# Optimization experiments

Hardware: AMD Instinct MI355X
Metric: run time of the kernel (lower is better)

Reference implementation:

```python
import math
import jax, jax.numpy as jnp
import numpy as np

NUM_HEADS = 16
D_MODEL = 1024
WINDOW = 512


def alibi_slopes(num_heads):
    # 1 / ((2**8)**((i+1)/num_heads))  for i in range(num_heads)
    x = (2.0 ** 8) ** (1.0 / num_heads)
    return jnp.asarray([1.0 / x ** (i + 1) for i in range(num_heads)], dtype=jnp.float32)


def setup_inputs() -> dict:
    key = jax.random.key(0)
    k1, k2 = jax.random.split(key)
    x = jax.random.normal(k1, (1, 4096, D_MODEL), dtype=jnp.float32)
    # scale weight like a trained init so softmax isn't saturated
    w_kqv = jax.random.normal(k2, (D_MODEL, 3 * D_MODEL), dtype=jnp.float32) * 0.02
    return {"x": x, "w_kqv": w_kqv}


def reference(x, w_kqv):
    B, S, D = x.shape
    H = NUM_HEADS
    hd = D // H
    scale = math.sqrt(D)  # module scales by sqrt(d_model), not sqrt(head_dim)

    kqv = x @ w_kqv                       # [B, S, 3D]
    k, q, v = jnp.split(kqv, 3, axis=-1)  # chunk order: key, query, value
    k = k.reshape(B, S, H, hd).transpose(0, 2, 1, 3)  # [B, H, S, hd]
    q = q.reshape(B, S, H, hd).transpose(0, 2, 1, 3)
    v = v.reshape(B, S, H, hd).transpose(0, 2, 1, 3)

    # ALiBi bias: m_h * (j - i)
    pos = jnp.arange(S)
    rel = pos[None, :] - pos[:, None]                  # [S, S] = x - y
    bias = alibi_slopes(H)[:, None, None] * rel.astype(jnp.float32)  # [H, S, S]

    score = jnp.einsum("bhqd,bhkd->bhqk", q, k) / scale + bias[None]

    # causal sliding-window mask: allow 0 <= i - j <= WINDOW
    dist = pos[:, None] - pos[None, :]                 # i - j
    mask = (dist >= 0) & (dist <= WINDOW)              # [S, S]
    score = jnp.where(mask[None, None], score, -jnp.inf)

    attn = jax.nn.softmax(score, axis=-1)
    out = jnp.einsum("bhqk,bhkd->bhqd", attn, v)       # [B, H, S, hd]
    out = out.transpose(0, 2, 1, 3).reshape(B, S, D)
    return out
```

## Files before the change

### kernel.cpp

```cpp
#include <hip/hip_runtime.h>
#include <hip/hip_bf16.h>

#define SEQ   4096
#define DM    1024
#define NH    16
#define HD    64
#define N3    3072
#define WIN   512

#define LOG2E 1.4426950408889634f

typedef __attribute__((ext_vector_type(8))) short short8;
typedef __attribute__((ext_vector_type(4))) short short4v;
typedef __attribute__((ext_vector_type(4))) float float4v;

__device__ __forceinline__ float bf16_bits_to_float(unsigned short u) {
  return __uint_as_float(((unsigned int)u) << 16);
}

typedef __attribute__((address_space(3))) void lds_void_t;
typedef __attribute__((address_space(1))) const void gbl_void_t;
__device__ __forceinline__ void async_copy16(void* lds_dst, const void* g_src) {
  __builtin_amdgcn_global_load_lds((gbl_void_t*)g_src, (lds_void_t*)lds_dst,
                                   16, 0, 0);
}

__device__ __forceinline__ int detect_fp32(const unsigned short* __restrict__ probe,
                                           float* red) {
  const int t = threadIdx.x;
  float mx = 0.0f;
#pragma unroll
  for (int p = 0; p < 8; ++p) {
    float v = bf16_bits_to_float(probe[(t * 8 + p) * 2]);
    if (v != v) v = 1e38f;
    mx = fmaxf(mx, fabsf(v));
  }
  red[t] = mx;
  __syncthreads();
  for (int s = 128; s > 0; s >>= 1) {
    if (t < s) red[t] = fmaxf(red[t], red[t + s]);
    __syncthreads();
  }
  const int fl = red[0] > 100.0f ? 1 : 0;
  __syncthreads();
  return fl;
}

__global__ __launch_bounds__(256) void prep(
    const void* __restrict__ x, const void* __restrict__ w,
    __hip_bfloat16* __restrict__ xb, __hip_bfloat16* __restrict__ wt) {
  __shared__ __hip_bfloat16 tile[64][66];
  __shared__ float red[256];
  const int t = threadIdx.x;
  if (blockIdx.x < 2048) {
    const int fl = detect_fp32((const unsigned short*)x, red);
    const int i0 = (blockIdx.x * 256 + t) * 8;
    if (fl) {
      const float* xf = (const float*)x + i0;
      float4 f0 = *(const float4*)(xf);
      float4 f1 = *(const float4*)(xf + 4);
      __hip_bfloat16 tmp[8];
      tmp[0] = __float2bfloat16(f0.x); tmp[1] = __float2bfloat16(f0.y);
      tmp[2] = __float2bfloat16(f0.z); tmp[3] = __float2bfloat16(f0.w);
      tmp[4] = __float2bfloat16(f1.x); tmp[5] = __float2bfloat16(f1.y);
      tmp[6] = __float2bfloat16(f1.z); tmp[7] = __float2bfloat16(f1.w);
      *(uint4*)&xb[i0] = *(const uint4*)tmp;
    } else {
      *(uint4*)&xb[i0] = *(const uint4*)((const __hip_bfloat16*)x + i0);
    }
  } else {
    const int bid = blockIdx.x - 2048;
    const int fl = detect_fp32((const unsigned short*)w, red);
    const int n0 = (bid % 48) * 64;
    const int k0 = (bid / 48) * 64;
    const int tx = t & 63, ty0 = t >> 6;
    if (fl) {
      const float* wf = (const float*)w;
#pragma unroll
      for (int p = 0; p < 16; ++p) {
        int row = ty0 + p * 4;
        tile[row][tx] = __float2bfloat16(wf[(k0 + row) * N3 + n0 + tx]);
      }
    } else {
      const __hip_bfloat16* wb = (const __hip_bfloat16*)w;
#pragma unroll
      for (int p = 0; p < 16; ++p) {
        int row = ty0 + p * 4;
        tile[row][tx] = wb[(k0 + row) * N3 + n0 + tx];
      }
    }
    __syncthreads();
#pragma unroll
    for (int r = 0; r < 2; ++r) {
      int oe = r * 2048 + t * 8;
      int nr = oe >> 6, kc = oe & 63;
      __hip_bfloat16 v[8];
#pragma unroll
      for (int e = 0; e < 8; ++e) v[e] = tile[kc + e][nr];
      *(uint4*)&wt[(n0 + nr) * DM + k0 + kc] = *(const uint4*)v;
    }
  }
}

__global__ __launch_bounds__(256) void gemm_kqv(
    const __hip_bfloat16* __restrict__ A,
    const __hip_bfloat16* __restrict__ BT,
    __hip_bfloat16* __restrict__ C) {
  __shared__ __align__(16) __hip_bfloat16 As[2][128 * 32];
  __shared__ __align__(16) __hip_bfloat16 Bs[2][128 * 32];
  const int m0 = blockIdx.y * 128;
  const int n0 = blockIdx.x * 128;
  const int t = threadIdx.x;
  const int wave = t >> 6, lane = t & 63;
  const int wm = wave >> 1, wn = wave & 1;
  const int l15 = lane & 15, quad = lane >> 4;

  const int srow0 = wave * 16 + (lane >> 2);
  const int scol  = (lane & 3) * 8;
  const int sbyte = wave * 1024 + lane * 16;

  float4v acc[4][4] = {};

  for (int k0 = 0; k0 < DM; k0 += 64) {
    __syncthreads();
#pragma unroll
    for (int half = 0; half < 2; ++half) {
      const int kk = k0 + half * 32;
#pragma unroll
      for (int r = 0; r < 2; ++r) {
        const int row = srow0 + r * 64;
        async_copy16((char*)As[half] + r * 4096 + sbyte,
                     &A[(m0 + row) * DM + kk + scol]);
        async_copy16((char*)Bs[half] + r * 4096 + sbyte,
                     &BT[(n0 + row) * DM + kk + scol]);
      }
    }
    __syncthreads();

#pragma unroll
    for (int half = 0; half < 2; ++half) {
      short8 a[4], b[4];
#pragma unroll
      for (int mi = 0; mi < 4; ++mi)
        a[mi] = *(const short8*)(&As[half][(wm * 64 + mi * 16 + l15) * 32 + quad * 8]);
#pragma unroll
      for (int ni = 0; ni < 4; ++ni)
        b[ni] = *(const short8*)(&Bs[half][(wn * 64 + ni * 16 + l15) * 32 + quad * 8]);
#pragma unroll
      for (int mi = 0; mi < 4; ++mi)
#pragma unroll
        for (int ni = 0; ni < 4; ++ni)
          acc[mi][ni] = __builtin_amdgcn_mfma_f32_16x16x32_bf16(
              a[mi], b[ni], acc[mi][ni], 0, 0, 0);
    }
  }

#pragma unroll
  for (int mi = 0; mi < 4; ++mi)
#pragma unroll
    for (int ni = 0; ni < 4; ++ni)
#pragma unroll
      for (int r = 0; r < 4; ++r) {
        int row = m0 + wm * 64 + mi * 16 + quad * 4 + r;
        int col = n0 + wn * 64 + ni * 16 + l15;
        C[row * N3 + col] = __float2bfloat16(acc[mi][ni][r]);
      }
}

__global__ __launch_bounds__(256, 4) void attn(
    const __hip_bfloat16* __restrict__ kqv,
    const unsigned short* __restrict__ xprobe,
    void* __restrict__ out) {
  __shared__ __align__(16) __hip_bfloat16 Ks[64 * 72];
  __shared__ __align__(16) __hip_bfloat16 Vt[80 * 68];
  __shared__ __align__(16) __hip_bfloat16 Ps[64 * 72];
  __shared__ float red[256];

  const int fl = detect_fp32(xprobe, red);
  const int h  = blockIdx.y;
  const int i0 = blockIdx.x * 64;
  const int t    = threadIdx.x;
  const int wave = t >> 6, lane = t & 63;
  const int l15 = lane & 15, quad = lane >> 4;
  const float slope2 = exp2f(-0.5f * (float)(h + 1)) * LOG2E;
  const float qscale = LOG2E / 32.0f;

  for (int idx = t; idx < 16 * 68; idx += 256) {
    int rr = idx / 68, cc = idx - rr * 68;
    ((unsigned short*)Vt)[(64 + rr) * 68 + cc] = (rr == 0) ? 0x3F80 : 0;
  }

  short8 aq[2];
#pragma unroll
  for (int ks2 = 0; ks2 < 2; ++ks2)
    aq[ks2] = *(const short8*)&kqv[(i0 + wave * 16 + l15) * N3 + DM + h * HD +
                                   ks2 * 32 + quad * 8];

  float4v o[5] = {};

  const int jlo  = max(0, i0 - WIN);
  const int nblk = (i0 + 64 - jlo) >> 6;

  for (int b = 0; b < nblk; ++b) {
    const int j0 = jlo + b * 64;
    __syncthreads();
    for (int c = t; c < 512; c += 256) {
      int row = c >> 3, d0 = (c & 7) * 8;
      *(uint4*)&Ks[row * 72 + d0] =
          *(const uint4*)&kqv[(j0 + row) * N3 + h * HD + d0];
    }
    {
      int rp = t >> 3, d0 = (t & 7) * 8, r0 = rp * 2;
      uint4 va = *(const uint4*)&kqv[(j0 + r0) * N3 + 2 * DM + h * HD + d0];
      uint4 vb = *(const uint4*)&kqv[(j0 + r0 + 1) * N3 + 2 * DM + h * HD + d0];
      const unsigned short* pa = (const unsigned short*)&va;
      const unsigned short* pb = (const unsigned short*)&vb;
#pragma unroll
      for (int e = 0; e < 8; ++e) {
        unsigned int pack = (unsigned int)pa[e] | ((unsigned int)pb[e] << 16);
        *(unsigned int*)&Vt[(d0 + e) * 68 + r0] = pack;
      }
    }
    __syncthreads();

    float4v sacc[4] = {};
#pragma unroll
    for (int ks2 = 0; ks2 < 2; ++ks2)
#pragma unroll
      for (int nt = 0; nt < 4; ++nt) {
        short8 bk = *(const short8*)&Ks[(nt * 16 + l15) * 72 + ks2 * 32 + quad * 8];
        sacc[nt] = __builtin_amdgcn_mfma_f32_16x16x32_bf16(aq[ks2], bk, sacc[nt], 0, 0, 0);
      }

#pragma unroll
    for (int r = 0; r < 4; ++r) {
      const int i = i0 + wave * 16 + quad * 4 + r;
#pragma unroll
      for (int nt = 0; nt < 4; ++nt) {
        const int j = j0 + nt * 16 + l15;
        const int rel = i - j;
        float x = sacc[nt][r] * qscale + slope2 * (float)(j - i);
        x = (rel >= 0 && rel <= WIN) ? x : -200.0f;
        Ps[(wave * 16 + quad * 4 + r) * 72 + nt * 16 + l15] =
            __float2bfloat16(exp2f(x));
      }
    }

#pragma unroll
    for (int ks = 0; ks < 64; ks += 32) {
      short8 ap = *(const short8*)&Ps[(wave * 16 + l15) * 72 + ks + quad * 8];
#pragma unroll
      for (int dt = 0; dt < 5; ++dt) {
        const __hip_bfloat16* vp = &Vt[(dt * 16 + l15) * 68 + ks + quad * 8];
        short4v v0 = *(const short4v*)vp;
        short4v v1 = *(const short4v*)(vp + 4);
        short8 bv;
#pragma unroll
        for (int e = 0; e < 4; ++e) { bv[e] = v0[e]; bv[4 + e] = v1[e]; }
        o[dt] = __builtin_amdgcn_mfma_f32_16x16x32_bf16(ap, bv, o[dt], 0, 0, 0);
      }
    }
  }

#pragma unroll
  for (int r = 0; r < 4; ++r) {
    const float l = __shfl(o[4][r], quad * 16, 64);
    const float inv_l = 1.0f / l;
    const int row = i0 + wave * 16 + quad * 4 + r;
#pragma unroll
    for (int dt = 0; dt < 4; ++dt) {
      const int idx = row * DM + h * HD + dt * 16 + l15;
      const float v = o[dt][r] * inv_l;
      if (fl) ((float*)out)[idx] = v;
      else    ((__hip_bfloat16*)out)[idx] = __float2bfloat16(v);
    }
  }
}

extern "C" void kernel_launch(void* const* d_in, const int* in_sizes, int n_in,
                              void* d_out, int out_size, void* d_ws, size_t ws_size,
                              hipStream_t stream) {
  char* ws = (char*)d_ws;
  __hip_bfloat16* wt  = (__hip_bfloat16*)(ws + 4096);
  __hip_bfloat16* kqv = (__hip_bfloat16*)(ws + 4096 + 6291456);
  __hip_bfloat16* xb  = (__hip_bfloat16*)d_out;

  hipLaunchKernelGGL(prep, dim3(2048 + 768), dim3(256), 0, stream,
                     d_in[0], d_in[1], xb, wt);
  hipLaunchKernelGGL(gemm_kqv, dim3(24, 32), dim3(256), 0, stream, xb, wt, kqv);
  hipLaunchKernelGGL(attn, dim3(64, 16), dim3(256), 0, stream,
                     kqv, (const unsigned short*)d_in[0], d_out);
}
```

Baseline: 152.0 us.

## Prefetch next K/V tile into registers and interleave query-block order

The attention loop now loads the next K and V tiles from global memory into registers while the current tile is being computed, so global latency overlaps with MFMA and softmax work. Query blocks are permuted across blockIdx.x to balance the uneven per-block work near the sequence start. The bias and mask math is strength-reduced to an incremental fmaf plus an unsigned compare, and the V fragment assembly uses a shufflevector. The register prefetch raises per-thread register use, which could lower occupancy under the launch bound of 4.

```diff
diff --git a/kernel.cpp b/kernel.cpp
--- a/kernel.cpp
+++ b/kernel.cpp
@@ -25,6 +25,7 @@
                                    16, 0, 0);
 }
 
+template <int NT>
 __device__ __forceinline__ int detect_fp32(const unsigned short* __restrict__ probe,
                                            float* red) {
   const int t = threadIdx.x;
@@ -37,7 +38,7 @@
   }
   red[t] = mx;
   __syncthreads();
-  for (int s = 128; s > 0; s >>= 1) {
+  for (int s = NT / 2; s > 0; s >>= 1) {
     if (t < s) red[t] = fmaxf(red[t], red[t + s]);
     __syncthreads();
   }
@@ -53,7 +54,7 @@
   __shared__ float red[256];
   const int t = threadIdx.x;
   if (blockIdx.x < 2048) {
-    const int fl = detect_fp32((const unsigned short*)x, red);
+    const int fl = detect_fp32<256>((const unsigned short*)x, red);
     const int i0 = (blockIdx.x * 256 + t) * 8;
     if (fl) {
       const float* xf = (const float*)x + i0;
@@ -70,7 +71,7 @@
     }
   } else {
     const int bid = blockIdx.x - 2048;
-    const int fl = detect_fp32((const unsigned short*)w, red);
+    const int fl = detect_fp32<256>((const unsigned short*)w, red);
     const int n0 = (bid % 48) * 64;
     const int k0 = (bid / 48) * 64;
     const int tx = t & 63, ty0 = t >> 6;
@@ -176,14 +177,16 @@
   __shared__ __align__(16) __hip_bfloat16 Ps[64 * 72];
   __shared__ float red[256];
 
-  const int fl = detect_fp32(xprobe, red);
+  const int fl = detect_fp32<256>(xprobe, red);
   const int h  = blockIdx.y;
-  const int i0 = blockIdx.x * 64;
+  const int bx = blockIdx.x;
+  const int i0 = 64 * ((bx & 7) * 8 + (bx >> 3));
   const int t    = threadIdx.x;
   const int wave = t >> 6, lane = t & 63;
   const int l15 = lane & 15, quad = lane >> 4;
-  const float slope2 = exp2f(-0.5f * (float)(h + 1)) * LOG2E;
-  const float qscale = LOG2E / 32.0f;
+  const float slope2  = exp2f(-0.5f * (float)(h + 1)) * LOG2E;
+  const float nslope2 = -slope2;
+  const float qscale  = LOG2E / 32.0f;
 
   for (int idx = t; idx < 16 * 68; idx += 256) {
     int rr = idx / 68, cc = idx - rr * 68;
@@ -201,25 +204,34 @@
   const int jlo  = max(0, i0 - WIN);
   const int nblk = (i0 + 64 - jlo) >> 6;
 
+  const int krow0 = t >> 3, krow1 = (t >> 3) + 32, kd0 = (t & 7) * 8;
+  const int vr0 = (t >> 3) * 2, vd0 = (t & 7) * 8;
+  uint4 kregA, kregB, vregA, vregB;
+  kregA = *(const uint4*)&kqv[(jlo + krow0) * N3 + h * HD + kd0];
+  kregB = *(const uint4*)&kqv[(jlo + krow1) * N3 + h * HD + kd0];
+  vregA = *(const uint4*)&kqv[(jlo + vr0) * N3 + 2 * DM + h * HD + vd0];
+  vregB = *(const uint4*)&kqv[(jlo + vr0 + 1) * N3 + 2 * DM + h * HD + vd0];
+
   for (int b = 0; b < nblk; ++b) {
     const int j0 = jlo + b * 64;
     __syncthreads();
-    for (int c = t; c < 512; c += 256) {
-      int row = c >> 3, d0 = (c & 7) * 8;
-      *(uint4*)&Ks[row * 72 + d0] =
-          *(const uint4*)&kqv[(j0 + row) * N3 + h * HD + d0];
-    }
+    *(uint4*)&Ks[krow0 * 72 + kd0] = kregA;
+    *(uint4*)&Ks[krow1 * 72 + kd0] = kregB;
     {
-      int rp = t >> 3, d0 = (t & 7) * 8, r0 = rp * 2;
-      uint4 va = *(const uint4*)&kqv[(j0 + r0) * N3 + 2 * DM + h * HD + d0];
-      uint4 vb = *(const uint4*)&kqv[(j0 + r0 + 1) * N3 + 2 * DM + h * HD + d0];
-      const unsigned short* pa = (const unsigned short*)&va;
-      const unsigned short* pb = (const unsigned short*)&vb;
+      const unsigned short* pa = (const unsigned short*)&vregA;
+      const unsigned short* pb = (const unsigned short*)&vregB;
 #pragma unroll
       for (int e = 0; e < 8; ++e) {
         unsigned int pack = (unsigned int)pa[e] | ((unsigned int)pb[e] << 16);
-        *(unsigned int*)&Vt[(d0 + e) * 68 + r0] = pack;
-      }
+        *(unsigned int*)&Vt[(vd0 + e) * 68 + vr0] = pack;
+      }
+    }
+    if (b + 1 < nblk) {
+      const int jn = j0 + 64;
+      kregA = *(const uint4*)&kqv[(jn + krow0) * N3 + h * HD + kd0];
+      kregB = *(const uint4*)&kqv[(jn + krow1) * N3 + h * HD + kd0];
+      vregA = *(const uint4*)&kqv[(jn + vr0) * N3 + 2 * DM + h * HD + vd0];
+      vregB = *(const uint4*)&kqv[(jn + vr0 + 1) * N3 + 2 * DM + h * HD + vd0];
     }
     __syncthreads();
 
@@ -232,17 +244,20 @@
         sacc[nt] = __builtin_amdgcn_mfma_f32_16x16x32_bf16(aq[ks2], bk, sacc[nt], 0, 0, 0);
       }
 
+    const int dbase = (i0 + wave * 16 + quad * 4) - (j0 + l15);
+    const float s16 = nslope2 * -16.0f;
 #pragma unroll
     for (int r = 0; r < 4; ++r) {
-      const int i = i0 + wave * 16 + quad * 4 + r;
+      float bias = nslope2 * (float)(dbase + r);
+      int rel = dbase + r;
 #pragma unroll
       for (int nt = 0; nt < 4; ++nt) {
-        const int j = j0 + nt * 16 + l15;
-        const int rel = i - j;
-        float x = sacc[nt][r] * qscale + slope2 * (float)(j - i);
-        x = (rel >= 0 && rel <= WIN) ? x : -200.0f;
+        float x = fmaf(sacc[nt][r], qscale, bias);
+        x = ((unsigned)rel <= (unsigned)WIN) ? x : -200.0f;
         Ps[(wave * 16 + quad * 4 + r) * 72 + nt * 16 + l15] =
             __float2bfloat16(exp2f(x));
+        bias += s16;
+        rel -= 16;
       }
     }
 
@@ -254,9 +269,7 @@
         const __hip_bfloat16* vp = &Vt[(dt * 16 + l15) * 68 + ks + quad * 8];
         short4v v0 = *(const short4v*)vp;
         short4v v1 = *(const short4v*)(vp + 4);
-        short8 bv;
-#pragma unroll
-        for (int e = 0; e < 4; ++e) { bv[e] = v0[e]; bv[4 + e] = v1[e]; }
+        short8 bv = __builtin_shufflevector(v0, v1, 0, 1, 2, 3, 4, 5, 6, 7);
         o[dt] = __builtin_amdgcn_mfma_f32_16x16x32_bf16(ap, bv, o[dt], 0, 0, 0);
       }
     }
```

Measured after the change: 148.9 us. 1.02x faster.
